# Optimization experiments

Hardware: AMD Instinct MI355X
Metric: run time of the kernel (lower is better)

The kernel has to match this reference:

```python
import jax, jax.numpy as jnp
import numpy as np

SOBEL_X = jnp.array([[1., 0., -1.], [2., 0., -2.], [1., 0., -1.]], dtype=jnp.float32).reshape(1, 1, 3, 3)
SOBEL_Y = jnp.array([[1., 2., 1.], [0., 0., 0.], [-1., -2., -1.]], dtype=jnp.float32).reshape(1, 1, 3, 3)
EPS = 1e-3


def _sobel(img, kern):
    # img: [N, 1, H, W]; 3x3 conv, zero padding 1 (torch Conv2d padding=1)
    return jax.lax.conv_general_dilated(
        img, kern, window_strides=(1, 1), padding='SAME',
        dimension_numbers=('NCHW', 'OIHW', 'NCHW'))


def _compute_flow(frames):
    # frames: [B, T, 3, H, W] -> flow: [B, T-1, 2, H, W]
    B, T, C, H, W = frames.shape
    gray = (0.2989 * frames[:, :, 0] + 0.587 * frames[:, :, 1]
            + 0.114 * frames[:, :, 2])  # [B, T, H, W]
    I1 = gray[:, :-1].reshape(B * (T - 1), 1, H, W)
    I2 = gray[:, 1:].reshape(B * (T - 1), 1, H, W)
    Ix = _sobel(I1, SOBEL_X)
    Iy = _sobel(I1, SOBEL_Y)
    It = I2 - I1
    denom = Ix * Ix + Iy * Iy + EPS
    u = -Ix * It / denom
    v = -Iy * It / denom
    return jnp.concatenate([u, v], axis=1).reshape(B, T - 1, 2, H, W)


def setup_inputs() -> dict:
    key = jax.random.key(0)
    k1, k2 = jax.random.split(key)
    shape = (8, 8, 3, 256, 256)  # [B, T, C, H, W]
    pred = jax.random.uniform(k1, shape, dtype=jnp.float32)
    gt = jax.random.uniform(k2, shape, dtype=jnp.float32)
    return {"pred": pred, "gt": gt}


def reference(pred, gt):
    pred_flow = _compute_flow(pred)  # [B, T-1, 2, H, W]
    gt_flow = _compute_flow(gt)
    # motion magnitude: mean abs frame diff over channels, broadcast over 2 flow channels
    motion_mag = jnp.abs(gt[:, 1:] - gt[:, :-1]).mean(axis=2, keepdims=True)  # [B, T-1, 1, H, W]
    flow_loss = (jnp.abs(pred_flow - gt_flow) * motion_mag).mean()
    return flow_loss
```

## Files before the change

### kernel.cpp

```cpp
#include <hip/hip_runtime.h>

#define BB 8
#define TT 8
#define HH 256
#define WW 256
#define PAIRS (BB * (TT - 1))
#define FRAME_PIX (HH * WW)
#define RROWS 8
#define HROWS (RROWS + 2)
#define PADW 264
#define NY (HH / RROWS)
#define NBLK (PAIRS * NY)
#define EPS 1e-3f
#define INV_N (1.0f / (float)((size_t)PAIRS * 2 * HH * WW))

__device__ __forceinline__ float4 ld4(const float* __restrict__ p) {
    return *reinterpret_cast<const float4*>(p);
}

__global__ __launch_bounds__(256) void flow_loss_kernel(
    const float* __restrict__ pred, const float* __restrict__ gt,
    float* __restrict__ partial)
{
    __shared__ float sg[2][HROWS][PADW];

    const int ytile = blockIdx.x;
    const int pair  = blockIdx.y;
    const int b = pair / (TT - 1);
    const int t = pair % (TT - 1);
    const size_t fs = (size_t)3 * FRAME_PIX;
    const float* p1 = pred + ((size_t)b * TT + t) * fs;
    const float* p2 = p1 + fs;
    const float* g1 = gt + ((size_t)b * TT + t) * fs;
    const float* g2 = g1 + fs;

    const int y0 = ytile * RROWS;
    const int tid = threadIdx.x;

    for (int i = tid; i < 2 * HROWS * 66; i += 256) {
        const int img = i / (HROWS * 66);
        const int rem = i - img * (HROWS * 66);
        const int row = rem / 66;
        const int p   = rem - row * 66;
        const int yr  = y0 - 1 + row;
        float vx = 0.f, vy = 0.f, vz = 0.f, vw = 0.f;
        if (p >= 1 && p <= 64 && (unsigned)yr < HH) {
            const float* base = img ? g1 : p1;
            const int off = yr * WW + (p - 1) * 4;
            const float4 r  = ld4(base + off);
            const float4 g  = ld4(base + off + FRAME_PIX);
            const float4 bl = ld4(base + off + 2 * FRAME_PIX);
            vx = 0.2989f * r.x + 0.587f * g.x + 0.114f * bl.x;
            vy = 0.2989f * r.y + 0.587f * g.y + 0.114f * bl.y;
            vz = 0.2989f * r.z + 0.587f * g.z + 0.114f * bl.z;
            vw = 0.2989f * r.w + 0.587f * g.w + 0.114f * bl.w;
        }
        float4 v; v.x = vx; v.y = vy; v.z = vz; v.w = vw;
        *reinterpret_cast<float4*>(&sg[img][row][p * 4]) = v;
    }
    __syncthreads();

    const int c4 = tid & 63;
    const int rb = tid >> 6;
    const int x  = c4 * 4;
    float s = 0.f;

    #pragma unroll
    for (int pass = 0; pass < 2; ++pass) {
        const int r   = pass * 4 + rb;
        const int y   = y0 + r;
        const int idx = y * WW + x;

        const float4 ar = ld4(g1 + idx), ag = ld4(g1 + idx + FRAME_PIX), ab = ld4(g1 + idx + 2 * FRAME_PIX);
        const float4 br = ld4(g2 + idx), bg = ld4(g2 + idx + FRAME_PIX), bb = ld4(g2 + idx + 2 * FRAME_PIX);
        const float4 cr = ld4(p2 + idx), cg = ld4(p2 + idx + FRAME_PIX), cb = ld4(p2 + idx + 2 * FRAME_PIX);

        float gp2[4], gg2[4], mm[4];
        gp2[0] = 0.2989f * cr.x + 0.587f * cg.x + 0.114f * cb.x;
        gp2[1] = 0.2989f * cr.y + 0.587f * cg.y + 0.114f * cb.y;
        gp2[2] = 0.2989f * cr.z + 0.587f * cg.z + 0.114f * cb.z;
        gp2[3] = 0.2989f * cr.w + 0.587f * cg.w + 0.114f * cb.w;
        gg2[0] = 0.2989f * br.x + 0.587f * bg.x + 0.114f * bb.x;
        gg2[1] = 0.2989f * br.y + 0.587f * bg.y + 0.114f * bb.y;
        gg2[2] = 0.2989f * br.z + 0.587f * bg.z + 0.114f * bb.z;
        gg2[3] = 0.2989f * br.w + 0.587f * bg.w + 0.114f * bb.w;
        mm[0] = (fabsf(br.x - ar.x) + fabsf(bg.x - ag.x) + fabsf(bb.x - ab.x)) * (1.0f / 3.0f);
        mm[1] = (fabsf(br.y - ar.y) + fabsf(bg.y - ag.y) + fabsf(bb.y - ab.y)) * (1.0f / 3.0f);
        mm[2] = (fabsf(br.z - ar.z) + fabsf(bg.z - ag.z) + fabsf(bb.z - ab.z)) * (1.0f / 3.0f);
        mm[3] = (fabsf(br.w - ar.w) + fabsf(bg.w - ag.w) + fabsf(bb.w - ab.w)) * (1.0f / 3.0f);

        float up[4], vp[4];
        #pragma unroll
        for (int img = 0; img < 2; ++img) {
            float w0[6], w1[6], w2[6];
            {
                const float* b0 = &sg[img][r][x];
                const float4 A = ld4(b0), B = ld4(b0 + 4), C = ld4(b0 + 8);
                w0[0] = A.w; w0[1] = B.x; w0[2] = B.y; w0[3] = B.z; w0[4] = B.w; w0[5] = C.x;
            }
            {
                const float* b1 = &sg[img][r + 1][x];
                const float4 A = ld4(b1), B = ld4(b1 + 4), C = ld4(b1 + 8);
                w1[0] = A.w; w1[1] = B.x; w1[2] = B.y; w1[3] = B.z; w1[4] = B.w; w1[5] = C.x;
            }
            {
                const float* b2 = &sg[img][r + 2][x];
                const float4 A = ld4(b2), B = ld4(b2 + 4), C = ld4(b2 + 8);
                w2[0] = A.w; w2[1] = B.x; w2[2] = B.y; w2[3] = B.z; w2[4] = B.w; w2[5] = C.x;
            }
            #pragma unroll
            for (int j = 0; j < 4; ++j) {
                const float Ix = (w0[j] - w0[j + 2]) + 2.0f * (w1[j] - w1[j + 2]) + (w2[j] - w2[j + 2]);
                const float Iy = (w0[j] + 2.0f * w0[j + 1] + w0[j + 2])
                               - (w2[j] + 2.0f * w2[j + 1] + w2[j + 2]);
                const float It = (img ? gg2[j] : gp2[j]) - w1[j + 1];
                const float d  = Ix * Ix + Iy * Iy + EPS;
                const float inv = 1.0f / d;
                if (img == 0) {
                    up[j] = -(Ix * It) * inv;
                    vp[j] = -(Iy * It) * inv;
                } else {
                    s += (fabsf(up[j] + (Ix * It) * inv) + fabsf(vp[j] + (Iy * It) * inv)) * mm[j];
                }
            }
        }
    }

    #pragma unroll
    for (int off = 32; off > 0; off >>= 1) s += __shfl_down(s, off, 64);

    __shared__ float wsum[4];
    if ((tid & 63) == 0) wsum[tid >> 6] = s;
    __syncthreads();
    if (tid == 0) {
        partial[pair * NY + ytile] = wsum[0] + wsum[1] + wsum[2] + wsum[3];
    }
}

__global__ __launch_bounds__(256) void reduce_kernel(
    const float* __restrict__ partial, float* __restrict__ out)
{
    float s = 0.0f;
    for (int i = threadIdx.x; i < NBLK / 4; i += 256) {
        const float4 v = ld4(partial + 4 * i);
        s += (v.x + v.y) + (v.z + v.w);
    }
    #pragma unroll
    for (int off = 32; off > 0; off >>= 1) s += __shfl_down(s, off, 64);

    __shared__ float wsum[4];
    if ((threadIdx.x & 63) == 0) wsum[threadIdx.x >> 6] = s;
    __syncthreads();
    if (threadIdx.x == 0) {
        out[0] = (wsum[0] + wsum[1] + wsum[2] + wsum[3]) * INV_N;
    }
}

extern "C" void kernel_launch(void* const* d_in, const int* in_sizes, int n_in,
                              void* d_out, int out_size, void* d_ws, size_t ws_size,
                              hipStream_t stream) {
    const float* pred = (const float*)d_in[0];
    const float* gt   = (const float*)d_in[1];
    float* partial    = (float*)d_ws;
    float* out        = (float*)d_out;

    dim3 grid(NY, PAIRS);
    dim3 block(256);
    flow_loss_kernel<<<grid, block, 0, stream>>>(pred, gt, partial);
    reduce_kernel<<<1, 256, 0, stream>>>(partial, out);
}
```

Before: 128.4 us.

## Stream consecutive frames per block to reuse grayscale and frame loads

Each block now covers a run of 3-4 consecutive frame pairs (the sequence split into two halves) instead of a single pair. The second frame's grayscale tile and its raw gt pixels are kept in shared memory and registers and reused as the first frame of the next pair, which cuts global traffic from roughly four frame reads per pair to about two. The costs are fewer blocks (512 instead of 1792), extra barriers per time step, higher register pressure under a 2-blocks-per-SIMD launch bound, and a loss of parallelism. The reduce kernel is also simplified to a fixed two loads per thread.

```diff
diff --git a/kernel.cpp b/kernel.cpp
--- a/kernel.cpp
+++ b/kernel.cpp
@@ -4,126 +4,191 @@
 #define TT 8
 #define HH 256
 #define WW 256
-#define PAIRS (BB * (TT - 1))
 #define FRAME_PIX (HH * WW)
 #define RROWS 8
-#define HROWS (RROWS + 2)
 #define PADW 264
 #define NY (HH / RROWS)
-#define NBLK (PAIRS * NY)
+#define NBLK (BB * 2 * NY)
 #define EPS 1e-3f
-#define INV_N (1.0f / (float)((size_t)PAIRS * 2 * HH * WW))
+#define INV_N (1.0f / (float)((size_t)BB * (TT - 1) * 2 * HH * WW))
 
 __device__ __forceinline__ float4 ld4(const float* __restrict__ p) {
     return *reinterpret_cast<const float4*>(p);
 }
 
-__global__ __launch_bounds__(256) void flow_loss_kernel(
+__device__ __forceinline__ float4 gray4(const float4 r, const float4 g, const float4 b) {
+    float4 o;
+    o.x = 0.2989f * r.x + 0.587f * g.x + 0.114f * b.x;
+    o.y = 0.2989f * r.y + 0.587f * g.y + 0.114f * b.y;
+    o.z = 0.2989f * r.z + 0.587f * g.z + 0.114f * b.z;
+    o.w = 0.2989f * r.w + 0.587f * g.w + 0.114f * b.w;
+    return o;
+}
+
+__global__ __launch_bounds__(256, 2) void flow_loss_kernel(
     const float* __restrict__ pred, const float* __restrict__ gt,
     float* __restrict__ partial)
 {
-    __shared__ float sg[2][HROWS][PADW];
+    __shared__ float gbuf[2][RROWS + 2][PADW];
 
     const int ytile = blockIdx.x;
-    const int pair  = blockIdx.y;
-    const int b = pair / (TT - 1);
-    const int t = pair % (TT - 1);
+    const int half  = blockIdx.y;
+    const int b     = blockIdx.z;
+    const int t0    = half * 4;
+    const int npair = half ? 3 : 4;
+    const int y0    = ytile * RROWS;
+    const int tid   = threadIdx.x;
     const size_t fs = (size_t)3 * FRAME_PIX;
-    const float* p1 = pred + ((size_t)b * TT + t) * fs;
-    const float* p2 = p1 + fs;
-    const float* g1 = gt + ((size_t)b * TT + t) * fs;
-    const float* g2 = g1 + fs;
-
-    const int y0 = ytile * RROWS;
-    const int tid = threadIdx.x;
-
-    for (int i = tid; i < 2 * HROWS * 66; i += 256) {
-        const int img = i / (HROWS * 66);
-        const int rem = i - img * (HROWS * 66);
-        const int row = rem / 66;
-        const int p   = rem - row * 66;
-        const int yr  = y0 - 1 + row;
-        float vx = 0.f, vy = 0.f, vz = 0.f, vw = 0.f;
-        if (p >= 1 && p <= 64 && (unsigned)yr < HH) {
-            const float* base = img ? g1 : p1;
-            const int off = yr * WW + (p - 1) * 4;
-            const float4 r  = ld4(base + off);
-            const float4 g  = ld4(base + off + FRAME_PIX);
-            const float4 bl = ld4(base + off + 2 * FRAME_PIX);
-            vx = 0.2989f * r.x + 0.587f * g.x + 0.114f * bl.x;
-            vy = 0.2989f * r.y + 0.587f * g.y + 0.114f * bl.y;
-            vz = 0.2989f * r.z + 0.587f * g.z + 0.114f * bl.z;
-            vw = 0.2989f * r.w + 0.587f * g.w + 0.114f * bl.w;
-        }
-        float4 v; v.x = vx; v.y = vy; v.z = vz; v.w = vw;
-        *reinterpret_cast<float4*>(&sg[img][row][p * 4]) = v;
+    const float* pb = pred + (size_t)b * TT * fs;
+    const float* gb = gt   + (size_t)b * TT * fs;
+
+    const int cx  = (tid & 63) * 4;
+    const int rb_ = tid >> 6;
+
+    const int h_img  = tid >> 7;
+    const int h_rsel = (tid >> 6) & 1;
+    const int h_x    = (tid & 63) * 4;
+    const int h_y    = h_rsel ? (y0 + RROWS) : (y0 - 1);
+    const bool h_ok  = ((unsigned)h_y) < HH;
+    const int h_brow = h_rsel ? (RROWS + 1) : 0;
+    const size_t h_off = h_ok ? ((size_t)h_y * WW + h_x) : 0;
+
+    if (tid < 160) {
+        const int img = tid / 80, rem = tid % 80, row = rem / 8, k = rem % 8;
+        const int col = (k < 4) ? k : (k + 256);
+        gbuf[img][row][col] = 0.f;
+    }
+
+    float4 g1c[2][3];
+
+    {
+        const float* p1 = pb + (size_t)t0 * fs;
+        const float* g1 = gb + (size_t)t0 * fs;
+        float4 pg[2], gg[2];
+        #pragma unroll
+        for (int pass = 0; pass < 2; ++pass) {
+            const int r = pass * 4 + rb_;
+            const size_t off = (size_t)(y0 + r) * WW + cx;
+            const float4 pr = ld4(p1 + off), pgc = ld4(p1 + off + FRAME_PIX),
+                         pbc = ld4(p1 + off + 2 * FRAME_PIX);
+            g1c[pass][0] = ld4(g1 + off);
+            g1c[pass][1] = ld4(g1 + off + FRAME_PIX);
+            g1c[pass][2] = ld4(g1 + off + 2 * FRAME_PIX);
+            pg[pass] = gray4(pr, pgc, pbc);
+            gg[pass] = gray4(g1c[pass][0], g1c[pass][1], g1c[pass][2]);
+        }
+        const float* hb = h_img ? g1 : p1;
+        float4 hg = make_float4(0.f, 0.f, 0.f, 0.f);
+        if (h_ok) {
+            const float4 r0 = ld4(hb + h_off), g0 = ld4(hb + h_off + FRAME_PIX),
+                         b0 = ld4(hb + h_off + 2 * FRAME_PIX);
+            hg = gray4(r0, g0, b0);
+        }
+        #pragma unroll
+        for (int pass = 0; pass < 2; ++pass) {
+            const int r = pass * 4 + rb_;
+            *reinterpret_cast<float4*>(&gbuf[0][r + 1][cx + 4]) = pg[pass];
+            *reinterpret_cast<float4*>(&gbuf[1][r + 1][cx + 4]) = gg[pass];
+        }
+        *reinterpret_cast<float4*>(&gbuf[h_img][h_brow][h_x + 4]) = hg;
     }
     __syncthreads();
 
-    const int c4 = tid & 63;
-    const int rb = tid >> 6;
-    const int x  = c4 * 4;
     float s = 0.f;
-
-    #pragma unroll
-    for (int pass = 0; pass < 2; ++pass) {
-        const int r   = pass * 4 + rb;
-        const int y   = y0 + r;
-        const int idx = y * WW + x;
-
-        const float4 ar = ld4(g1 + idx), ag = ld4(g1 + idx + FRAME_PIX), ab = ld4(g1 + idx + 2 * FRAME_PIX);
-        const float4 br = ld4(g2 + idx), bg = ld4(g2 + idx + FRAME_PIX), bb = ld4(g2 + idx + 2 * FRAME_PIX);
-        const float4 cr = ld4(p2 + idx), cg = ld4(p2 + idx + FRAME_PIX), cb = ld4(p2 + idx + 2 * FRAME_PIX);
-
-        float gp2[4], gg2[4], mm[4];
-        gp2[0] = 0.2989f * cr.x + 0.587f * cg.x + 0.114f * cb.x;
-        gp2[1] = 0.2989f * cr.y + 0.587f * cg.y + 0.114f * cb.y;
-        gp2[2] = 0.2989f * cr.z + 0.587f * cg.z + 0.114f * cb.z;
-        gp2[3] = 0.2989f * cr.w + 0.587f * cg.w + 0.114f * cb.w;
-        gg2[0] = 0.2989f * br.x + 0.587f * bg.x + 0.114f * bb.x;
-        gg2[1] = 0.2989f * br.y + 0.587f * bg.y + 0.114f * bb.y;
-        gg2[2] = 0.2989f * br.z + 0.587f * bg.z + 0.114f * bb.z;
-        gg2[3] = 0.2989f * br.w + 0.587f * bg.w + 0.114f * bb.w;
-        mm[0] = (fabsf(br.x - ar.x) + fabsf(bg.x - ag.x) + fabsf(bb.x - ab.x)) * (1.0f / 3.0f);
-        mm[1] = (fabsf(br.y - ar.y) + fabsf(bg.y - ag.y) + fabsf(bb.y - ab.y)) * (1.0f / 3.0f);
-        mm[2] = (fabsf(br.z - ar.z) + fabsf(bg.z - ag.z) + fabsf(bb.z - ab.z)) * (1.0f / 3.0f);
-        mm[3] = (fabsf(br.w - ar.w) + fabsf(bg.w - ag.w) + fabsf(bb.w - ab.w)) * (1.0f / 3.0f);
-
-        float up[4], vp[4];
-        #pragma unroll
-        for (int img = 0; img < 2; ++img) {
-            float w0[6], w1[6], w2[6];
-            {
-                const float* b0 = &sg[img][r][x];
-                const float4 A = ld4(b0), B = ld4(b0 + 4), C = ld4(b0 + 8);
-                w0[0] = A.w; w0[1] = B.x; w0[2] = B.y; w0[3] = B.z; w0[4] = B.w; w0[5] = C.x;
+    for (int t = t0; t < t0 + npair; ++t) {
+        const float* p2 = pb + (size_t)(t + 1) * fs;
+        const float* g2 = gb + (size_t)(t + 1) * fs;
+
+        float4 p2c[2][3], g2c[2][3];
+        #pragma unroll
+        for (int pass = 0; pass < 2; ++pass) {
+            const int r = pass * 4 + rb_;
+            const size_t off = (size_t)(y0 + r) * WW + cx;
+            p2c[pass][0] = ld4(p2 + off);
+            p2c[pass][1] = ld4(p2 + off + FRAME_PIX);
+            p2c[pass][2] = ld4(p2 + off + 2 * FRAME_PIX);
+            g2c[pass][0] = ld4(g2 + off);
+            g2c[pass][1] = ld4(g2 + off + FRAME_PIX);
+            g2c[pass][2] = ld4(g2 + off + 2 * FRAME_PIX);
+        }
+        const float* hb = h_img ? g2 : p2;
+        float4 hgray = make_float4(0.f, 0.f, 0.f, 0.f);
+        if (h_ok) {
+            const float4 r0 = ld4(hb + h_off), g0 = ld4(hb + h_off + FRAME_PIX),
+                         b0 = ld4(hb + h_off + 2 * FRAME_PIX);
+            hgray = gray4(r0, g0, b0);
+        }
+
+        float4 gp2[2], gg2[2];
+        #pragma unroll
+        for (int pass = 0; pass < 2; ++pass) {
+            gp2[pass] = gray4(p2c[pass][0], p2c[pass][1], p2c[pass][2]);
+            gg2[pass] = gray4(g2c[pass][0], g2c[pass][1], g2c[pass][2]);
+        }
+
+        #pragma unroll
+        for (int pass = 0; pass < 2; ++pass) {
+            const int r = pass * 4 + rb_;
+            float mm[4];
+            mm[0] = (fabsf(g2c[pass][0].x - g1c[pass][0].x) + fabsf(g2c[pass][1].x - g1c[pass][1].x)
+                   + fabsf(g2c[pass][2].x - g1c[pass][2].x)) * (1.f / 3.f);
+            mm[1] = (fabsf(g2c[pass][0].y - g1c[pass][0].y) + fabsf(g2c[pass][1].y - g1c[pass][1].y)
+                   + fabsf(g2c[pass][2].y - g1c[pass][2].y)) * (1.f / 3.f);
+            mm[2] = (fabsf(g2c[pass][0].z - g1c[pass][0].z) + fabsf(g2c[pass][1].z - g1c[pass][1].z)
+                   + fabsf(g2c[pass][2].z - g1c[pass][2].z)) * (1.f / 3.f);
+            mm[3] = (fabsf(g2c[pass][0].w - g1c[pass][0].w) + fabsf(g2c[pass][1].w - g1c[pass][1].w)
+                   + fabsf(g2c[pass][2].w - g1c[pass][2].w)) * (1.f / 3.f);
+
+            float up[4], vp[4];
+            #pragma unroll
+            for (int img = 0; img < 2; ++img) {
+                float w0[6], w1[6], w2[6];
+                {
+                    const float* p = &gbuf[img][r][cx];
+                    const float4 A = ld4(p), B = ld4(p + 4), C = ld4(p + 8);
+                    w0[0] = A.w; w0[1] = B.x; w0[2] = B.y; w0[3] = B.z; w0[4] = B.w; w0[5] = C.x;
+                }
+                {
+                    const float* p = &gbuf[img][r + 1][cx];
+                    const float4 A = ld4(p), B = ld4(p + 4), C = ld4(p + 8);
+                    w1[0] = A.w; w1[1] = B.x; w1[2] = B.y; w1[3] = B.z; w1[4] = B.w; w1[5] = C.x;
+                }
+                {
+                    const float* p = &gbuf[img][r + 2][cx];
+                    const float4 A = ld4(p), B = ld4(p + 4), C = ld4(p + 8);
+                    w2[0] = A.w; w2[1] = B.x; w2[2] = B.y; w2[3] = B.z; w2[4] = B.w; w2[5] = C.x;
+                }
+                const float4 gr2 = img ? gg2[pass] : gp2[pass];
+                const float g2a[4] = {gr2.x, gr2.y, gr2.z, gr2.w};
+                #pragma unroll
+                for (int j = 0; j < 4; ++j) {
+                    const float Ix = (w0[j] - w0[j + 2]) + 2.0f * (w1[j] - w1[j + 2]) + (w2[j] - w2[j + 2]);
+                    const float Iy = (w0[j] + 2.0f * w0[j + 1] + w0[j + 2])
+                                   - (w2[j] + 2.0f * w2[j + 1] + w2[j + 2]);
+                    const float It = g2a[j] - w1[j + 1];
+                    const float inv = 1.0f / (Ix * Ix + Iy * Iy + EPS);
+                    if (img == 0) {
+                        up[j] = -(Ix * It) * inv;
+                        vp[j] = -(Iy * It) * inv;
+                    } else {
+                        s += (fabsf(up[j] + (Ix * It) * inv) + fabsf(vp[j] + (Iy * It) * inv)) * mm[j];
+                    }
+                }
             }
-            {
-                const float* b1 = &sg[img][r + 1][x];
-                const float4 A = ld4(b1), B = ld4(b1 + 4), C = ld4(b1 + 8);
-                w1[0] = A.w; w1[1] = B.x; w1[2] = B.y; w1[3] = B.z; w1[4] = B.w; w1[5] = C.x;
-            }
-            {
-                const float* b2 = &sg[img][r + 2][x];
-                const float4 A = ld4(b2), B = ld4(b2 + 4), C = ld4(b2 + 8);
-                w2[0] = A.w; w2[1] = B.x; w2[2] = B.y; w2[3] = B.z; w2[4] = B.w; w2[5] = C.x;
-            }
-            #pragma unroll
-            for (int j = 0; j < 4; ++j) {
-                const float Ix = (w0[j] - w0[j + 2]) + 2.0f * (w1[j] - w1[j + 2]) + (w2[j] - w2[j + 2]);
-                const float Iy = (w0[j] + 2.0f * w0[j + 1] + w0[j + 2])
-                               - (w2[j] + 2.0f * w2[j + 1] + w2[j + 2]);
-                const float It = (img ? gg2[j] : gp2[j]) - w1[j + 1];
-                const float d  = Ix * Ix + Iy * Iy + EPS;
-                const float inv = 1.0f / d;
-                if (img == 0) {
-                    up[j] = -(Ix * It) * inv;
-                    vp[j] = -(Iy * It) * inv;
-                } else {
-                    s += (fabsf(up[j] + (Ix * It) * inv) + fabsf(vp[j] + (Iy * It) * inv)) * mm[j];
-                }
-            }
-        }
+        }
+        __syncthreads();
+
+        #pragma unroll
+        for (int pass = 0; pass < 2; ++pass) {
+            const int r = pass * 4 + rb_;
+            *reinterpret_cast<float4*>(&gbuf[0][r + 1][cx + 4]) = gp2[pass];
+            *reinterpret_cast<float4*>(&gbuf[1][r + 1][cx + 4]) = gg2[pass];
+            g1c[pass][0] = g2c[pass][0];
+            g1c[pass][1] = g2c[pass][1];
+            g1c[pass][2] = g2c[pass][2];
+        }
+        *reinterpret_cast<float4*>(&gbuf[h_img][h_brow][h_x + 4]) = hgray;
+        __syncthreads();
     }
 
     #pragma unroll
@@ -133,18 +198,14 @@
     if ((tid & 63) == 0) wsum[tid >> 6] = s;
     __syncthreads();
     if (tid == 0) {
-        partial[pair * NY + ytile] = wsum[0] + wsum[1] + wsum[2] + wsum[3];
+        partial[(b * 2 + half) * NY + ytile] = wsum[0] + wsum[1] + wsum[2] + wsum[3];
     }
 }
 
 __global__ __launch_bounds__(256) void reduce_kernel(
     const float* __restrict__ partial, float* __restrict__ out)
 {
-    float s = 0.0f;
-    for (int i = threadIdx.x; i < NBLK / 4; i += 256) {
-        const float4 v = ld4(partial + 4 * i);
-        s += (v.x + v.y) + (v.z + v.w);
-    }
+    float s = partial[threadIdx.x] + partial[threadIdx.x + 256];
     #pragma unroll
     for (int off = 32; off > 0; off >>= 1) s += __shfl_down(s, off, 64);
 
@@ -164,7 +225,7 @@
     float* partial    = (float*)d_ws;
     float* out        = (float*)d_out;
 
-    dim3 grid(NY, PAIRS);
+    dim3 grid(NY, 2, BB);
     dim3 block(256);
     flow_loss_kernel<<<grid, block, 0, stream>>>(pred, gt, partial);
     reduce_kernel<<<1, 256, 0, stream>>>(partial, out);
```

New measurement: 122.1 us. -5.0%, faster.
